# Kernel optimization log

Hardware: AMD Instinct MI355X
Metric: run time of the kernel (lower is better)

The kernel has to match this reference:

```python
import jax, jax.numpy as jnp
import numpy as np

NUM_GRAPHS = 128
EPS = 1e-5


def _instance_norm(x, seg):
    # per-graph (segment) normalization over rows, per channel; affine=False (PyG default)
    ones = jnp.ones((x.shape[0],), x.dtype)
    cnt = jnp.maximum(jax.ops.segment_sum(ones, seg, num_segments=NUM_GRAPHS), 1.0)[:, None]
    mean = jax.ops.segment_sum(x, seg, num_segments=NUM_GRAPHS) / cnt
    ex2 = jax.ops.segment_sum(x * x, seg, num_segments=NUM_GRAPHS) / cnt
    var = jnp.maximum(ex2 - mean * mean, 0.0)
    return (x - mean[seg]) * jax.lax.rsqrt(var[seg] + EPS)


def setup_inputs() -> dict:
    key = jax.random.key(0)
    ks = jax.random.split(key, 6)
    N, E, H = 100_000, 1_600_000, 64
    emb = jax.random.normal(ks[0], (N, H), jnp.float32)
    edge_index = jax.random.randint(ks[1], (2, E), 0, N)
    batch = jnp.sort(jax.random.randint(ks[2], (N,), 0, NUM_GRAPHS))
    s = lambda fan: 1.0 / np.sqrt(fan)
    # MLP layers [2H, 4H, H, 1]
    W1 = jax.random.uniform(ks[3], (2 * H, 4 * H), jnp.float32, -s(2 * H), s(2 * H))
    b1 = jnp.zeros((4 * H,), jnp.float32)
    W2 = jax.random.uniform(ks[4], (4 * H, H), jnp.float32, -s(4 * H), s(4 * H))
    b2 = jnp.zeros((H,), jnp.float32)
    W3 = jax.random.uniform(ks[5], (H, 1), jnp.float32, -s(H), s(H))
    b3 = jnp.zeros((1,), jnp.float32)
    return dict(emb=emb, edge_index=edge_index, batch=batch,
                W1=W1, b1=b1, W2=W2, b2=b2, W3=W3, b3=b3)


def reference(emb, edge_index, batch, W1, b1, W2, b2, W3, b3):
    col, row = edge_index[0], edge_index[1]
    # edge-wise gather + concat: [E, 2H]
    f12 = jnp.concatenate([emb[col], emb[row]], axis=-1)
    seg = batch[col]  # graph id per edge
    h = jax.nn.relu(_instance_norm(f12 @ W1 + b1, seg))   # [E, 4H]
    h = jax.nn.relu(_instance_norm(h @ W2 + b2, seg))     # [E, H]
    att_log_logits = h @ W3 + b3                          # [E, 1]
    return att_log_logits
```

## Files before the change

kernel.cpp:

```cpp
#include <hip/hip_runtime.h>
#include <hip/hip_bf16.h>

#define NSEG 128
#define H64 64
#define C1 256
#define K1 128
#define C2 64
#define EPSV 1e-5f
#define NWG 256

typedef __attribute__((ext_vector_type(8))) short bf16x8;
typedef __attribute__((ext_vector_type(16))) float f32x16;
typedef __attribute__((ext_vector_type(4))) unsigned int u32x4;

struct BTrue  { static constexpr bool value = true; };
struct BFalse { static constexpr bool value = false; };

__device__ __forceinline__ unsigned short f2bf(float f){
  unsigned int x = __float_as_uint(f);
  x += 0x7fffu + ((x >> 16) & 1u);
  return (unsigned short)(x >> 16);
}
__device__ __forceinline__ float bf2f(unsigned short u){
  return __uint_as_float(((unsigned int)u) << 16);
}
__device__ __forceinline__ unsigned pkbf(float lo, float hi){
  unsigned r;
  asm("v_cvt_pk_bf16_f32 %0, %1, %2" : "=v"(r) : "v"(lo), "v"(hi));
  return r;
}
__device__ __forceinline__ bf16x8 mk8(unsigned a, unsigned b, unsigned c, unsigned d){
  u32x4 t = {a, b, c, d};
  return __builtin_bit_cast(bf16x8, t);
}
__device__ __forceinline__ int xcd_swz(int bid, int nwg){
  int q = nwg >> 3, r = nwg & 7;
  int x = bid & 7, o = bid >> 3;
  return (x < r ? x * (q + 1) : r * (q + 1) + (x - r) * q) + o;
}

__global__ void k_cvt_emb(const float* __restrict__ src, unsigned short* __restrict__ dst, int n4){
  int i = blockIdx.x * blockDim.x + threadIdx.x;
  if (i >= n4) return;
  float4 v = ((const float4*)src)[i];
  unsigned int a = (unsigned int)f2bf(v.x) | ((unsigned int)f2bf(v.y) << 16);
  unsigned int b = (unsigned int)f2bf(v.z) | ((unsigned int)f2bf(v.w) << 16);
  ((uint2*)dst)[i] = make_uint2(a, b);
}

__global__ void k_cvt_w(const float* __restrict__ W1, const float* __restrict__ W2,
                        unsigned short* __restrict__ W1T, unsigned short* __restrict__ W2T){
  int i = blockIdx.x * blockDim.x + threadIdx.x;
  if (i < C1 * K1){
    int c = i >> 7, k = i & 127;
    W1T[i] = f2bf(W1[k * C1 + c]);
  } else {
    int j = i - C1 * K1;
    if (j < C2 * C1){
      int c = j >> 8, k = j & 255;
      W2T[j] = f2bf(W2[k * C2 + c]);
    }
  }
}

__global__ void k_hist(const int* __restrict__ col, const int* __restrict__ batch,
                       int* __restrict__ segE, int* __restrict__ cnt, int E){
  __shared__ int h[NSEG];
  for (int i = threadIdx.x; i < NSEG; i += blockDim.x) h[i] = 0;
  __syncthreads();
  int stride = gridDim.x * blockDim.x;
  for (int e = blockIdx.x * blockDim.x + threadIdx.x; e < E; e += stride){
    int s = batch[col[e]];
    segE[e] = s;
    atomicAdd(&h[s], 1);
  }
  __syncthreads();
  for (int i = threadIdx.x; i < NSEG; i += blockDim.x)
    if (h[i]) atomicAdd(&cnt[i], h[i]);
}

__global__ void k_scan(const int* __restrict__ cnt, int* __restrict__ cursor,
                       float* __restrict__ cntf){
  if (threadIdx.x == 0){
    int acc = 0;
    for (int i = 0; i < NSEG; i++){ cursor[i] = acc; acc += cnt[i]; }
  }
  if (threadIdx.x < NSEG){
    int c = cnt[threadIdx.x];
    cntf[threadIdx.x] = (float)(c > 0 ? c : 1);
  }
}

__global__ void k_scatter(const int* __restrict__ segE, const int* __restrict__ ei,
                          int* __restrict__ cursor, int* __restrict__ perm,
                          int* __restrict__ segS, int* __restrict__ ecol, int* __restrict__ erow,
                          int* __restrict__ invp, int E, int epb){
  __shared__ int h[NSEG];
  __shared__ int base[NSEG];
  int b0 = blockIdx.x * epb;
  int b1 = b0 + epb < E ? b0 + epb : E;
  for (int i = threadIdx.x; i < NSEG; i += blockDim.x) h[i] = 0;
  __syncthreads();
  for (int e = b0 + threadIdx.x; e < b1; e += blockDim.x) atomicAdd(&h[segE[e]], 1);
  __syncthreads();
  for (int i = threadIdx.x; i < NSEG; i += blockDim.x)
    base[i] = h[i] ? atomicAdd(&cursor[i], h[i]) : 0;
  __syncthreads();
  for (int i = threadIdx.x; i < NSEG; i += blockDim.x) h[i] = 0;
  __syncthreads();
  for (int e = b0 + threadIdx.x; e < b1; e += blockDim.x){
    int s = segE[e];
    int p = base[s] + atomicAdd(&h[s], 1);
    perm[p] = e; segS[p] = s;
    ecol[p] = ei[e]; erow[p] = ei[(size_t)E + e];
    invp[e] = p;
  }
}

__global__ void __launch_bounds__(1024, 4)
k_stats1(const unsigned short* __restrict__ ebf, const unsigned short* __restrict__ W1T,
         const int* __restrict__ ecol, const int* __restrict__ erow, const int* __restrict__ segS,
         float* __restrict__ sum1, float* __restrict__ sq1, int NWT, int E, int T)
{
  __shared__ __align__(16) char wl[65536];
  {
    #pragma unroll
    for (int j = 0; j < 4; j++){
      int i = threadIdx.x + j * 1024;
      int r = i >> 4, u = i & 15;
      u32x4 v = *(const u32x4*)(W1T + (size_t)r * K1 + u * 8);
      *(u32x4*)(wl + r * 256 + ((u ^ (r & 15)) << 4)) = v;
    }
  }
  __syncthreads();

  const int lane = threadIdx.x & 63, w = threadIdx.x >> 6;
  const int g = lane >> 5, l31 = lane & 31;
  const int bid = xcd_swz(blockIdx.x, NWG);
  const int wt0 = (bid * 16 + w) * T;
  float psum[8] = {0,0,0,0,0,0,0,0}, psq[8] = {0,0,0,0,0,0,0,0};
  int cur = -1;

  auto flush = [&](int seg){
    if (seg < 0) return;
    #pragma unroll
    for (int nt = 0; nt < 8; nt++){
      float sv = psum[nt] + __shfl_xor(psum[nt], 32);
      float qv = psq[nt]  + __shfl_xor(psq[nt], 32);
      if (lane < 32){
        atomicAdd(&sum1[seg * C1 + nt * 32 + l31], sv);
        atomicAdd(&sq1 [seg * C1 + nt * 32 + l31], qv);
      }
      psum[nt] = 0.f; psq[nt] = 0.f;
    }
  };

  auto ld3 = [&](int wt, int& a, int& r, int& s){
    int e = wt * 32 + l31;
    int ec = e < E ? e : E - 1;
    a = ecol[ec]; r = erow[ec]; s = segS[ec];
  };

  int cA, rA, sg;
  if (wt0 < NWT) ld3(wt0, cA, rA, sg);

  for (int it = 0; it < T; ++it){
    int wt = wt0 + it;
    if (wt >= NWT) break;
    const int p0 = wt * 32;
    int nA, nR, nS;
    const bool hv = (it + 1 < T) && (wt + 1 < NWT);
    if (hv) ld3(wt + 1, nA, nR, nS);

    bf16x8 fa[8];
    #pragma unroll
    for (int kk = 0; kk < 8; kk++){
      int off = (kk & 3) * 16 + g * 8;
      fa[kk] = *(const bf16x8*)(ebf + (size_t)(kk < 4 ? cA : rA) * H64 + off);
    }

    int sA = __builtin_amdgcn_readfirstlane(__shfl(sg, 0));
    int sB = __builtin_amdgcn_readfirstlane(__shfl(sg, 31));
    bool uni = (sA == sB) && (p0 + 32 <= E);
    if (uni && sA != cur){ flush(cur); cur = sA; }
    if (!uni){ flush(cur); cur = -1; }

    #pragma unroll 1
    for (int np = 0; np < 4; np++){
      const int nt0 = 2 * np, nt1 = 2 * np + 1;
      f32x16 a0, a1;
      #pragma unroll
      for (int r = 0; r < 16; r++){ a0[r] = 0.f; a1[r] = 0.f; }
      const int rw0 = nt0 * 32 + l31, rw1 = nt1 * 32 + l31;
      __builtin_amdgcn_s_setprio(1);
      #pragma unroll
      for (int kk = 0; kk < 8; kk++){
        bf16x8 b0 = *(const bf16x8*)(wl + rw0 * 256 + (((2 * kk + g) ^ (rw0 & 15)) << 4));
        bf16x8 b1 = *(const bf16x8*)(wl + rw1 * 256 + (((2 * kk + g) ^ (rw1 & 15)) << 4));
        a0 = __builtin_amdgcn_mfma_f32_32x32x16_bf16(fa[kk], b0, a0, 0, 0, 0);
        a1 = __builtin_amdgcn_mfma_f32_32x32x16_bf16(fa[kk], b1, a1, 0, 0, 0);
      }
      __builtin_amdgcn_s_setprio(0);
      if (uni){
        float t0 = 0.f, q0 = 0.f, t1 = 0.f, q1 = 0.f;
        #pragma unroll
        for (int r = 0; r < 16; r++){
          t0 += a0[r]; q0 += a0[r] * a0[r];
          t1 += a1[r]; q1 += a1[r] * a1[r];
        }
        psum[nt0] += t0; psq[nt0] += q0;
        psum[nt1] += t1; psq[nt1] += q1;
      } else {
        for (int s = sA; s <= sB; s++){
          float t0 = 0.f, q0 = 0.f, t1 = 0.f, q1 = 0.f;
          #pragma unroll
          for (int r = 0; r < 16; r++){
            int c = (r & 3) + 8 * (r >> 2) + 4 * g;
            bool ok = (__shfl(sg, c) == s) && (p0 + c < E);
            float v0 = ok ? a0[r] : 0.f;
            float v1 = ok ? a1[r] : 0.f;
            t0 += v0; q0 += v0 * v0;
            t1 += v1; q1 += v1 * v1;
          }
          float s0 = t0 + __shfl_xor(t0, 32);
          float qq0 = q0 + __shfl_xor(q0, 32);
          float s1 = t1 + __shfl_xor(t1, 32);
          float qq1 = q1 + __shfl_xor(q1, 32);
          if (lane < 32){
            atomicAdd(&sum1[s * C1 + nt0 * 32 + l31], s0);
            atomicAdd(&sq1 [s * C1 + nt0 * 32 + l31], qq0);
            atomicAdd(&sum1[s * C1 + nt1 * 32 + l31], s1);
            atomicAdd(&sq1 [s * C1 + nt1 * 32 + l31], qq1);
          }
        }
      }
    }
    if (hv){ cA = nA; rA = nR; sg = nS; }
  }
  flush(cur);
}

__global__ void k_fin(const float* __restrict__ sum, const float* __restrict__ sq,
                      const float* __restrict__ cntf,
                      float* __restrict__ sc, float* __restrict__ sh, int C){
  int i = blockIdx.x * blockDim.x + threadIdx.x;
  if (i >= NSEG * C) return;
  int s = i / C;
  float c = cntf[s];
  float m = sum[i] / c;
  float v = fmaxf(sq[i] / c - m * m, 0.f);
  float inv = rsqrtf(v + EPSV);
  sc[i] = inv;
  sh[i] = -m * inv;
}

template<int MODE>
__global__ void __launch_bounds__(1024, 4)
k_mid(const unsigned short* __restrict__ ebf, const unsigned short* __restrict__ W1T,
      const unsigned short* __restrict__ W2T,
      const int* __restrict__ ecol, const int* __restrict__ erow,
      const int* __restrict__ segS, const int* __restrict__ perm,
      const float* __restrict__ sc1, const float* __restrict__ sh1,
      float* __restrict__ sum2, float* __restrict__ sq2,
      unsigned int* __restrict__ y2u,
      const float* __restrict__ sc2, const float* __restrict__ sh2,
      const float* __restrict__ W3, const float* __restrict__ b3,
      float* __restrict__ out, int NWT, int E, int T)
{
  __shared__ __align__(16) char wl[98304];
  __shared__ __align__(16) float scsh[16][512];
  {
    #pragma unroll
    for (int j = 0; j < 4; j++){
      int i = threadIdx.x + j * 1024;
      int r = i >> 4, u = i & 15;
      u32x4 v = *(const u32x4*)(W1T + (size_t)r * K1 + u * 8);
      *(u32x4*)(wl + r * 256 + ((u ^ (r & 15)) << 4)) = v;
    }
    #pragma unroll
    for (int j = 0; j < 2; j++){
      int i = threadIdx.x + j * 1024;
      int r = i >> 5, u = i & 31;
      u32x4 v = *(const u32x4*)(W2T + (size_t)r * C1 + u * 8);
      *(u32x4*)(wl + 65536 + r * 512 + ((u ^ (r & 31)) << 4)) = v;
    }
  }
  __syncthreads();

  const int lane = threadIdx.x & 63, w = threadIdx.x >> 6;
  const int g = lane >> 5, l31 = lane & 31;
  const int bid = xcd_swz(blockIdx.x, NWG);
  const int wt0 = (bid * 16 + w) * T;

  float b3v = 0.f;
  if (MODE == 2) b3v = b3[0];
  int wseg = -1;
  float ps2[2] = {0.f, 0.f}, pq2[2] = {0.f, 0.f};
  int cur2 = -1;

  auto flush2 = [&](int seg){
    if (seg < 0) return;
    #pragma unroll
    for (int ct = 0; ct < 2; ct++){
      float sv = ps2[ct] + __shfl_xor(ps2[ct], 32);
      float qv = pq2[ct] + __shfl_xor(pq2[ct], 32);
      if (lane < 32){
        atomicAdd(&sum2[seg * C2 + ct * 32 + l31], sv);
        atomicAdd(&sq2 [seg * C2 + ct * 32 + l31], qv);
      }
      ps2[ct] = 0.f; pq2[ct] = 0.f;
    }
  };

  auto body = [&](auto uni_c, const bf16x8* fbp, int sgn, f32x16* acc2){
    constexpr bool UNI = decltype(uni_c)::value;
    #pragma unroll 1
    for (int mt = 0; mt < 8; mt++){
      f32x16 a1;
      #pragma unroll
      for (int r = 0; r < 16; r++) a1[r] = 0.f;
      const int rw = mt * 32 + l31;
      __builtin_amdgcn_s_setprio(1);
      #pragma unroll
      for (int kk = 0; kk < 8; kk++){
        bf16x8 wa = *(const bf16x8*)(wl + rw * 256 + (((2 * kk + g) ^ (rw & 15)) << 4));
        a1 = __builtin_amdgcn_mfma_f32_32x32x16_bf16(wa, fbp[kk], a1, 0, 0, 0);
      }
      __builtin_amdgcn_s_setprio(0);
      unsigned pk_[8];
      #pragma unroll
      for (int rq = 0; rq < 4; rq++){
        float4 sc, sh;
        if constexpr (UNI){
          sc = *(const float4*)(&scsh[w][mt * 32 + rq * 8 + 4 * g]);
          sh = *(const float4*)(&scsh[w][256 + mt * 32 + rq * 8 + 4 * g]);
        } else {
          sc = *(const float4*)(sc1 + sgn * C1 + mt * 32 + rq * 8 + 4 * g);
          sh = *(const float4*)(sh1 + sgn * C1 + mt * 32 + rq * 8 + 4 * g);
        }
        float h0 = fmaxf(fmaf(a1[rq * 4 + 0], sc.x, sh.x), 0.f);
        float h1 = fmaxf(fmaf(a1[rq * 4 + 1], sc.y, sh.y), 0.f);
        float h2 = fmaxf(fmaf(a1[rq * 4 + 2], sc.z, sh.z), 0.f);
        float h3 = fmaxf(fmaf(a1[rq * 4 + 3], sc.w, sh.w), 0.f);
        pk_[rq * 2 + 0] = pkbf(h0, h1);
        pk_[rq * 2 + 1] = pkbf(h2, h3);
      }
      asm("v_permlane32_swap_b32 %0, %1" : "+v"(pk_[0]), "+v"(pk_[2]));
      asm("v_permlane32_swap_b32 %0, %1" : "+v"(pk_[1]), "+v"(pk_[3]));
      asm("v_permlane32_swap_b32 %0, %1" : "+v"(pk_[4]), "+v"(pk_[6]));
      asm("v_permlane32_swap_b32 %0, %1" : "+v"(pk_[5]), "+v"(pk_[7]));
      bf16x8 bf0 = mk8(pk_[0], pk_[1], pk_[2], pk_[3]);
      bf16x8 bf1 = mk8(pk_[4], pk_[5], pk_[6], pk_[7]);
      __builtin_amdgcn_s_setprio(1);
      #pragma unroll
      for (int ct = 0; ct < 2; ct++){
        int rb = ct * 32 + l31;
        bf16x8 wb0 = *(const bf16x8*)(wl + 65536 + rb * 512 + (((4 * mt + g) ^ (rb & 31)) << 4));
        bf16x8 wb1 = *(const bf16x8*)(wl + 65536 + rb * 512 + (((4 * mt + 2 + g) ^ (rb & 31)) << 4));
        acc2[ct] = __builtin_amdgcn_mfma_f32_32x32x16_bf16(bf0, wb0, acc2[ct], 0, 0, 0);
        acc2[ct] = __builtin_amdgcn_mfma_f32_32x32x16_bf16(bf1, wb1, acc2[ct], 0, 0, 0);
      }
      __builtin_amdgcn_s_setprio(0);
    }
  };

  auto ld3 = [&](int wt, int& a, int& r, int& s){
    int e = wt * 32 + l31;
    int ec = e < E ? e : E - 1;
    a = ecol[ec]; r = erow[ec]; s = segS[ec];
  };

  int cA, rA, sg;
  if (wt0 < NWT) ld3(wt0, cA, rA, sg);

  for (int it = 0; it < T; ++it){
    int wt = wt0 + it;
    if (wt >= NWT) break;
    const int p0 = wt * 32;
    int nA, nR, nS;
    const bool hv = (it + 1 < T) && (wt + 1 < NWT);
    if (hv) ld3(wt + 1, nA, nR, nS);

    bf16x8 fb[8];
    #pragma unroll
    for (int kk = 0; kk < 8; kk++){
      int off = (kk & 3) * 16 + g * 8;
      fb[kk] = *(const bf16x8*)(ebf + (size_t)(kk < 4 ? cA : rA) * H64 + off);
    }

    int sA = __builtin_amdgcn_readfirstlane(__shfl(sg, 0));
    int sB = __builtin_amdgcn_readfirstlane(__shfl(sg, 31));
    const bool uni = (sA == sB) && (p0 + 32 <= E);

    if (uni && sA != wseg){
      float4 s4 = *(const float4*)(sc1 + sA * C1 + lane * 4);
      float4 h4 = *(const float4*)(sh1 + sA * C1 + lane * 4);
      *(float4*)(&scsh[w][lane * 4]) = s4;
      *(float4*)(&scsh[w][256 + lane * 4]) = h4;
      wseg = sA;
    }

    f32x16 acc2[2];
    #pragma unroll
    for (int ct = 0; ct < 2; ct++)
      #pragma unroll
      for (int r = 0; r < 16; r++) acc2[ct][r] = 0.f;

    if (uni) body(BTrue{},  fb, sg, acc2);
    else     body(BFalse{}, fb, sg, acc2);

    if constexpr (MODE < 2){
      if constexpr (MODE == 0){
        unsigned short* y2s = (unsigned short*)y2u;
        #pragma unroll
        for (int ct = 0; ct < 2; ct++){
          int ch = ct * 32 + l31;
          #pragma unroll
          for (int r = 0; r < 16; r++){
            int eloc = (r & 3) + 8 * (r >> 2) + 4 * g;
            if (p0 + eloc < E)
              y2s[(size_t)(p0 + eloc) * C2 + ch] = f2bf(acc2[ct][r]);
          }
        }
      }
      if (uni){
        if (sA != cur2){ flush2(cur2); cur2 = sA; }
        #pragma unroll
        for (int ct = 0; ct < 2; ct++){
          float ts = 0.f, tq = 0.f;
          #pragma unroll
          for (int r = 0; r < 16; r++){ float x = acc2[ct][r]; ts += x; tq += x * x; }
          ps2[ct] += ts; pq2[ct] += tq;
        }
      } else {
        flush2(cur2); cur2 = -1;
        for (int s = sA; s <= sB; s++){
          #pragma unroll
          for (int ct = 0; ct < 2; ct++){
            float ts = 0.f, tq = 0.f;
            #pragma unroll
            for (int r = 0; r < 16; r++){
              int eloc = (r & 3) + 8 * (r >> 2) + 4 * g;
              bool ok = (__shfl(sg, eloc) == s) && (p0 + eloc < E);
              float x = ok ? acc2[ct][r] : 0.f;
              ts += x; tq += x * x;
            }
            float sv = ts + __shfl_xor(ts, 32);
            float qv = tq + __shfl_xor(tq, 32);
            if (lane < 32){
              atomicAdd(&sum2[s * C2 + ct * 32 + l31], sv);
              atomicAdd(&sq2 [s * C2 + ct * 32 + l31], qv);
            }
          }
        }
      }
    } else {
      #pragma unroll
      for (int r = 0; r < 16; r++){
        int eloc = (r & 3) + 8 * (r >> 2) + 4 * g;
        int sge = uni ? sA : __shfl(sg, eloc);
        float vtot = 0.f;
        #pragma unroll
        for (int ct = 0; ct < 2; ct++){
          int ch = ct * 32 + l31;
          float scv = sc2[sge * C2 + ch], shv = sh2[sge * C2 + ch];
          vtot += fmaxf(fmaf(acc2[ct][r], scv, shv), 0.f) * W3[ch];
        }
        vtot += __shfl_xor(vtot, 1); vtot += __shfl_xor(vtot, 2);
        vtot += __shfl_xor(vtot, 4); vtot += __shfl_xor(vtot, 8); vtot += __shfl_xor(vtot, 16);
        if (l31 == 0 && p0 + eloc < E) out[perm[p0 + eloc]] = vtot + b3v;
      }
    }
    if (hv){ cA = nA; rA = nR; sg = nS; }
  }
  if constexpr (MODE < 2) flush2(cur2);
}

__global__ void k_out(const unsigned short* __restrict__ y2, const int* __restrict__ segS,
                      const float* __restrict__ sc2, const float* __restrict__ sh2,
                      const float* __restrict__ W3, const float* __restrict__ b3,
                      float* __restrict__ tmp, int E)
{
  const int lane = threadIdx.x & 63;
  const int wid = (blockIdx.x * blockDim.x + threadIdx.x) >> 6;
  const int nw = (gridDim.x * blockDim.x) >> 6;
  const int es = lane >> 3;
  const int cp = (lane & 7) * 8;
  float w3r[8];
  #pragma unroll
  for (int j = 0; j < 8; j++) w3r[j] = W3[cp + j];
  const float b3v = b3[0];
  for (long base = (long)wid * 8; base < E; base += (long)nw * 8){
    int pos = (int)base + es;
    float a = 0.f;
    if (pos < E){
      bf16x8 v = *(const bf16x8*)(y2 + (size_t)pos * C2 + cp);
      int s = segS[pos];
      const float* scp = sc2 + s * C2 + cp;
      const float* shp = sh2 + s * C2 + cp;
      #pragma unroll
      for (int j = 0; j < 8; j++){
        float hv = fmaxf(fmaf(bf2f((unsigned short)v[j]), scp[j], shp[j]), 0.f);
        a = fmaf(hv, w3r[j], a);
      }
    }
    a += __shfl_xor(a, 1); a += __shfl_xor(a, 2); a += __shfl_xor(a, 4);
    if ((lane & 7) == 0 && pos < E) tmp[pos] = a + b3v;
  }
}

__global__ void k_remap(const float* __restrict__ tmp, const int* __restrict__ invp,
                        float* __restrict__ out, int E)
{
  int stride = gridDim.x * blockDim.x;
  for (int e = blockIdx.x * blockDim.x + threadIdx.x; e < E; e += stride)
    out[e] = tmp[invp[e]];
}

extern "C" void kernel_launch(void* const* d_in, const int* in_sizes, int n_in,
                              void* d_out, int out_size, void* d_ws, size_t ws_size,
                              hipStream_t stream)
{
  const float* emb   = (const float*)d_in[0];
  const int*   ei    = (const int*)d_in[1];
  const int*   batch = (const int*)d_in[2];
  const float* W1    = (const float*)d_in[3];
  const float* W2    = (const float*)d_in[5];
  const float* W3    = (const float*)d_in[7];
  const float* b3    = (const float*)d_in[8];
  float* out = (float*)d_out;
  const int E = in_sizes[1] / 2;
  const int N = in_sizes[0] / H64;
  const int NWT = (E + 31) / 32;

  char* ws = (char*)d_ws;
  size_t o = 0;
  auto al = [&](size_t b){ size_t r = o; o = (o + b + 255) & ~((size_t)255); return r; };
  size_t o_ebf  = al((size_t)N * H64 * 2);
  size_t o_w1t  = al((size_t)C1 * K1 * 2);
  size_t o_w2t  = al((size_t)C2 * C1 * 2);
  size_t o_perm = al((size_t)E * 4);
  size_t o_segS = al((size_t)E * 4);
  size_t o_ecol = al((size_t)E * 4);
  size_t o_erow = al((size_t)E * 4);
  size_t o_invp = al((size_t)E * 4);
  size_t o_cnt  = al(NSEG * 4);
  size_t o_cur  = al(NSEG * 4);
  size_t o_cntf = al(NSEG * 4);
  size_t o_sum1 = al((size_t)NSEG * C1 * 4);
  size_t o_sq1  = al((size_t)NSEG * C1 * 4);
  size_t o_sum2 = al((size_t)NSEG * C2 * 4);
  size_t o_sq2  = al((size_t)NSEG * C2 * 4);
  size_t o_sc1  = al((size_t)NSEG * C1 * 4);
  size_t o_sh1  = al((size_t)NSEG * C1 * 4);
  size_t o_sc2  = al((size_t)NSEG * C2 * 4);
  size_t o_sh2  = al((size_t)NSEG * C2 * 4);
  size_t o_segE = al((size_t)E * 4);
  size_t o_y2   = o_segE;
  size_t need_full = o_segE + (size_t)E * C2 * 2;
  const bool full = ws_size >= need_full;

  unsigned short* ebf = (unsigned short*)(ws + o_ebf);
  unsigned short* W1T = (unsigned short*)(ws + o_w1t);
  unsigned short* W2T = (unsigned short*)(ws + o_w2t);
  int* perm = (int*)(ws + o_perm);
  int* segS = (int*)(ws + o_segS);
  int* ecol = (int*)(ws + o_ecol);
  int* erow = (int*)(ws + o_erow);
  int* invp = (int*)(ws + o_invp);
  int* cnt  = (int*)(ws + o_cnt);
  int* curp = (int*)(ws + o_cur);
  float* cntf = (float*)(ws + o_cntf);
  float* sum1 = (float*)(ws + o_sum1);
  float* sq1  = (float*)(ws + o_sq1);
  float* sum2 = (float*)(ws + o_sum2);
  float* sq2  = (float*)(ws + o_sq2);
  float* sc1  = (float*)(ws + o_sc1);
  float* sh1  = (float*)(ws + o_sh1);
  float* sc2  = (float*)(ws + o_sc2);
  float* sh2  = (float*)(ws + o_sh2);
  int* segE = (int*)(ws + o_segE);
  unsigned int* y2u = (unsigned int*)(ws + o_y2);
  unsigned short* y2 = (unsigned short*)(ws + o_y2);
  float* tmp = (float*)(ws + o_ecol);

  hipMemsetAsync(ws + o_cnt, 0, o_sc1 - o_cnt, stream);

  k_cvt_emb<<<(N * H64 / 4 + 255) / 256, 256, 0, stream>>>(emb, ebf, N * H64 / 4);
  k_cvt_w<<<192, 256, 0, stream>>>(W1, W2, W1T, W2T);

  k_hist<<<2048, 256, 0, stream>>>(ei, batch, segE, cnt, E);
  k_scan<<<1, 128, 0, stream>>>(cnt, curp, cntf);
  const int epb = 2048;
  k_scatter<<<(E + epb - 1) / epb, 256, 0, stream>>>(segE, ei, curp, perm, segS, ecol, erow, invp, E, epb);

  const int T = (NWT + NWG * 16 - 1) / (NWG * 16);
  k_stats1<<<NWG, 1024, 0, stream>>>(ebf, W1T, ecol, erow, segS, sum1, sq1, NWT, E, T);
  k_fin<<<(NSEG * C1) / 256, 256, 0, stream>>>(sum1, sq1, cntf, sc1, sh1, C1);

  if (full){
    k_mid<0><<<NWG, 1024, 0, stream>>>(ebf, W1T, W2T, ecol, erow, segS, perm,
        sc1, sh1, sum2, sq2, y2u, sc2, sh2, W3, b3, out, NWT, E, T);
    k_fin<<<(NSEG * C2) / 256, 256, 0, stream>>>(sum2, sq2, cntf, sc2, sh2, C2);
    k_out<<<1024, 256, 0, stream>>>(y2, segS, sc2, sh2, W3, b3, tmp, E);
    k_remap<<<2048, 256, 0, stream>>>(tmp, invp, out, E);
  } else {
    k_mid<1><<<NWG, 1024, 0, stream>>>(ebf, W1T, W2T, ecol, erow, segS, perm,
        sc1, sh1, sum2, sq2, nullptr, sc2, sh2, W3, b3, out, NWT, E, T);
    k_fin<<<(NSEG * C2) / 256, 256, 0, stream>>>(sum2, sq2, cntf, sc2, sh2, C2);
    k_mid<2><<<NWG, 1024, 0, stream>>>(ebf, W1T, W2T, ecol, erow, segS, perm,
        sc1, sh1, sum2, sq2, nullptr, sc2, sh2, W3, b3, out, NWT, E, T);
  }
}
```

Before: 565.6 us.

## Process 64 edges per wave tile in stats1 and merge conversion kernels

The first-layer statistics kernel now handles two 32-edge row blocks per wave iteration, so each W1 fragment read from LDS feeds two MFMAs instead of one, and the per-column sums are combined across both blocks. The next-tile index prefetch is dropped in favour of loading both blocks' indices directly. The embedding and weight bf16 conversion kernels are merged into one launch. The change trades fewer LDS reads for more registers per lane and the loss of index prefetch, which could hurt occupancy or latency hiding.

```diff
diff --git a/kernel.cpp b/kernel.cpp
--- a/kernel.cpp
+++ b/kernel.cpp
@@ -39,23 +39,24 @@
   return (x < r ? x * (q + 1) : r * (q + 1) + (x - r) * q) + o;
 }
 
-__global__ void k_cvt_emb(const float* __restrict__ src, unsigned short* __restrict__ dst, int n4){
+__global__ void k_cvt(const float* __restrict__ emb, const float* __restrict__ W1,
+                      const float* __restrict__ W2, unsigned short* __restrict__ ebf,
+                      unsigned short* __restrict__ W1T, unsigned short* __restrict__ W2T,
+                      int n4){
   int i = blockIdx.x * blockDim.x + threadIdx.x;
-  if (i >= n4) return;
-  float4 v = ((const float4*)src)[i];
-  unsigned int a = (unsigned int)f2bf(v.x) | ((unsigned int)f2bf(v.y) << 16);
-  unsigned int b = (unsigned int)f2bf(v.z) | ((unsigned int)f2bf(v.w) << 16);
-  ((uint2*)dst)[i] = make_uint2(a, b);
-}
-
-__global__ void k_cvt_w(const float* __restrict__ W1, const float* __restrict__ W2,
-                        unsigned short* __restrict__ W1T, unsigned short* __restrict__ W2T){
-  int i = blockIdx.x * blockDim.x + threadIdx.x;
-  if (i < C1 * K1){
-    int c = i >> 7, k = i & 127;
-    W1T[i] = f2bf(W1[k * C1 + c]);
+  if (i < n4){
+    float4 v = ((const float4*)emb)[i];
+    unsigned int a = (unsigned int)f2bf(v.x) | ((unsigned int)f2bf(v.y) << 16);
+    unsigned int b = (unsigned int)f2bf(v.z) | ((unsigned int)f2bf(v.w) << 16);
+    ((uint2*)ebf)[i] = make_uint2(a, b);
+    return;
+  }
+  int ip = i - n4;
+  if (ip < C1 * K1){
+    int c = ip >> 7, k = ip & 127;
+    W1T[ip] = f2bf(W1[k * C1 + c]);
   } else {
-    int j = i - C1 * K1;
+    int j = ip - C1 * K1;
     if (j < C2 * C1){
       int c = j >> 8, k = j & 255;
       W2T[j] = f2bf(W2[k * C2 + c]);
@@ -155,87 +156,72 @@
     }
   };
 
-  auto ld3 = [&](int wt, int& a, int& r, int& s){
-    int e = wt * 32 + l31;
-    int ec = e < E ? e : E - 1;
-    a = ecol[ec]; r = erow[ec]; s = segS[ec];
-  };
-
-  int cA, rA, sg;
-  if (wt0 < NWT) ld3(wt0, cA, rA, sg);
-
   for (int it = 0; it < T; ++it){
     int wt = wt0 + it;
     if (wt >= NWT) break;
-    const int p0 = wt * 32;
-    int nA, nR, nS;
-    const bool hv = (it + 1 < T) && (wt + 1 < NWT);
-    if (hv) ld3(wt + 1, nA, nR, nS);
-
-    bf16x8 fa[8];
+    const int p0 = wt * 64;
+    int e0 = p0 + l31, e1 = p0 + 32 + l31;
+    int e0c = e0 < E ? e0 : E - 1, e1c = e1 < E ? e1 : E - 1;
+    int cA = ecol[e0c], rA = erow[e0c], sg0 = segS[e0c];
+    int cB = ecol[e1c], rB = erow[e1c], sg1 = segS[e1c];
+
+    bf16x8 fa[2][8];
     #pragma unroll
     for (int kk = 0; kk < 8; kk++){
       int off = (kk & 3) * 16 + g * 8;
-      fa[kk] = *(const bf16x8*)(ebf + (size_t)(kk < 4 ? cA : rA) * H64 + off);
-    }
-
-    int sA = __builtin_amdgcn_readfirstlane(__shfl(sg, 0));
-    int sB = __builtin_amdgcn_readfirstlane(__shfl(sg, 31));
-    bool uni = (sA == sB) && (p0 + 32 <= E);
+      fa[0][kk] = *(const bf16x8*)(ebf + (size_t)(kk < 4 ? cA : rA) * H64 + off);
+      fa[1][kk] = *(const bf16x8*)(ebf + (size_t)(kk < 4 ? cB : rB) * H64 + off);
+    }
+
+    int sA = __builtin_amdgcn_readfirstlane(__shfl(sg0, 0));
+    int sB = __builtin_amdgcn_readfirstlane(__shfl(sg1, 31));
+    bool uni = (sA == sB) && (p0 + 64 <= E);
     if (uni && sA != cur){ flush(cur); cur = sA; }
     if (!uni){ flush(cur); cur = -1; }
 
     #pragma unroll 1
-    for (int np = 0; np < 4; np++){
-      const int nt0 = 2 * np, nt1 = 2 * np + 1;
+    for (int nt = 0; nt < 8; nt++){
       f32x16 a0, a1;
       #pragma unroll
       for (int r = 0; r < 16; r++){ a0[r] = 0.f; a1[r] = 0.f; }
-      const int rw0 = nt0 * 32 + l31, rw1 = nt1 * 32 + l31;
+      const int rw = nt * 32 + l31;
       __builtin_amdgcn_s_setprio(1);
       #pragma unroll
       for (int kk = 0; kk < 8; kk++){
-        bf16x8 b0 = *(const bf16x8*)(wl + rw0 * 256 + (((2 * kk + g) ^ (rw0 & 15)) << 4));
-        bf16x8 b1 = *(const bf16x8*)(wl + rw1 * 256 + (((2 * kk + g) ^ (rw1 & 15)) << 4));
-        a0 = __builtin_amdgcn_mfma_f32_32x32x16_bf16(fa[kk], b0, a0, 0, 0, 0);
-        a1 = __builtin_amdgcn_mfma_f32_32x32x16_bf16(fa[kk], b1, a1, 0, 0, 0);
+        bf16x8 b = *(const bf16x8*)(wl + rw * 256 + (((2 * kk + g) ^ (rw & 15)) << 4));
+        a0 = __builtin_amdgcn_mfma_f32_32x32x16_bf16(fa[0][kk], b, a0, 0, 0, 0);
+        a1 = __builtin_amdgcn_mfma_f32_32x32x16_bf16(fa[1][kk], b, a1, 0, 0, 0);
       }
       __builtin_amdgcn_s_setprio(0);
       if (uni){
-        float t0 = 0.f, q0 = 0.f, t1 = 0.f, q1 = 0.f;
+        float ts = 0.f, tq = 0.f;
         #pragma unroll
         for (int r = 0; r < 16; r++){
-          t0 += a0[r]; q0 += a0[r] * a0[r];
-          t1 += a1[r]; q1 += a1[r] * a1[r];
+          ts += a0[r] + a1[r];
+          tq += a0[r] * a0[r] + a1[r] * a1[r];
         }
-        psum[nt0] += t0; psq[nt0] += q0;
-        psum[nt1] += t1; psq[nt1] += q1;
+        psum[nt] += ts; psq[nt] += tq;
       } else {
         for (int s = sA; s <= sB; s++){
-          float t0 = 0.f, q0 = 0.f, t1 = 0.f, q1 = 0.f;
+          float ts = 0.f, tq = 0.f;
           #pragma unroll
           for (int r = 0; r < 16; r++){
             int c = (r & 3) + 8 * (r >> 2) + 4 * g;
-            bool ok = (__shfl(sg, c) == s) && (p0 + c < E);
-            float v0 = ok ? a0[r] : 0.f;
-            float v1 = ok ? a1[r] : 0.f;
-            t0 += v0; q0 += v0 * v0;
-            t1 += v1; q1 += v1 * v1;
+            bool ok0 = (__shfl(sg0, c) == s) && (p0 + c < E);
+            bool ok1 = (__shfl(sg1, c) == s) && (p0 + 32 + c < E);
+            float v0 = ok0 ? a0[r] : 0.f;
+            float v1 = ok1 ? a1[r] : 0.f;
+            ts += v0 + v1; tq += v0 * v0 + v1 * v1;
           }
-          float s0 = t0 + __shfl_xor(t0, 32);
-          float qq0 = q0 + __shfl_xor(q0, 32);
-          float s1 = t1 + __shfl_xor(t1, 32);
-          float qq1 = q1 + __shfl_xor(q1, 32);
+          float sv = ts + __shfl_xor(ts, 32);
+          float qv = tq + __shfl_xor(tq, 32);
           if (lane < 32){
-            atomicAdd(&sum1[s * C1 + nt0 * 32 + l31], s0);
-            atomicAdd(&sq1 [s * C1 + nt0 * 32 + l31], qq0);
-            atomicAdd(&sum1[s * C1 + nt1 * 32 + l31], s1);
-            atomicAdd(&sq1 [s * C1 + nt1 * 32 + l31], qq1);
+            atomicAdd(&sum1[s * C1 + nt * 32 + l31], sv);
+            atomicAdd(&sq1 [s * C1 + nt * 32 + l31], qv);
           }
         }
       }
     }
-    if (hv){ cA = nA; rA = nR; sg = nS; }
   }
   flush(cur);
 }
@@ -531,7 +517,8 @@
   float* out = (float*)d_out;
   const int E = in_sizes[1] / 2;
   const int N = in_sizes[0] / H64;
-  const int NWT = (E + 31) / 32;
+  const int NWT  = (E + 31) / 32;
+  const int NWT1 = (E + 63) / 64;
 
   char* ws = (char*)d_ws;
   size_t o = 0;
@@ -586,18 +573,19 @@
 
   hipMemsetAsync(ws + o_cnt, 0, o_sc1 - o_cnt, stream);
 
-  k_cvt_emb<<<(N * H64 / 4 + 255) / 256, 256, 0, stream>>>(emb, ebf, N * H64 / 4);
-  k_cvt_w<<<192, 256, 0, stream>>>(W1, W2, W1T, W2T);
+  const int n4 = N * H64 / 4;
+  k_cvt<<<(n4 + C1 * K1 + C2 * C1 + 255) / 256, 256, 0, stream>>>(emb, W1, W2, ebf, W1T, W2T, n4);
 
   k_hist<<<2048, 256, 0, stream>>>(ei, batch, segE, cnt, E);
   k_scan<<<1, 128, 0, stream>>>(cnt, curp, cntf);
   const int epb = 2048;
   k_scatter<<<(E + epb - 1) / epb, 256, 0, stream>>>(segE, ei, curp, perm, segS, ecol, erow, invp, E, epb);
 
+  const int T1 = (NWT1 + NWG * 16 - 1) / (NWG * 16);
+  k_stats1<<<NWG, 1024, 0, stream>>>(ebf, W1T, ecol, erow, segS, sum1, sq1, NWT1, E, T1);
+  k_fin<<<(NSEG * C1) / 256, 256, 0, stream>>>(sum1, sq1, cntf, sc1, sh1, C1);
+
   const int T = (NWT + NWG * 16 - 1) / (NWG * 16);
-  k_stats1<<<NWG, 1024, 0, stream>>>(ebf, W1T, ecol, erow, segS, sum1, sq1, NWT, E, T);
-  k_fin<<<(NSEG * C1) / 256, 256, 0, stream>>>(sum1, sq1, cntf, sc1, sh1, C1);
-
   if (full){
     k_mid<0><<<NWG, 1024, 0, stream>>>(ebf, W1T, W2T, ecol, erow, segS, perm,
         sc1, sh1, sum2, sq2, y2u, sc2, sh2, W3, b3, out, NWT, E, T);
```

After: 695.3 us. 1.23x slower.
